# Performance work log

Hardware: AMD Instinct MI355X
Metric: run time of the kernel (lower is better)

## Reference

```python
import jax, jax.numpy as jnp
import numpy as np

KE = 14.3996
R_MAX = 6.0
N_ATOMS = 100000
N_EDGES = 6400000

def _isp(x):
    # inverse softplus on host constants
    return np.log(np.exp(np.asarray(x, np.float64)) - 1.0).astype(np.float32)

def setup_inputs() -> dict:
    key = jax.random.key(0)
    k1, k2, k3 = jax.random.split(key, 3)
    R = jax.random.normal(k1, (N_ATOMS, 3), dtype=jnp.float32) * 10.0
    Z = jax.random.randint(k2, (N_ATOMS,), 1, 50, dtype=jnp.int32)
    idx = jax.random.randint(k3, (2, N_EDGES), 0, N_ATOMS, dtype=jnp.int32)
    return {
        "R": R,
        "Z": Z,
        "idx": idx,
        "a_exp": jnp.full((1,), _isp(0.23)),
        "a_num": jnp.full((1,), _isp(0.4685)),
        "coefficients": jnp.asarray(_isp([0.18175, 0.50986, 0.28022, 0.02817]))[:, None],
        "exponents": jnp.asarray(_isp([3.1998, 0.94229, 0.4029, 0.20162]))[:, None],
        "rep_scale": jnp.full((1,), _isp(1.0 / KE)),
    }

def reference(R, Z, idx, a_exp, a_num, coefficients, exponents, rep_scale):
    idx_i, idx_j = idx[0], idx[1]
    Zf = Z.astype(jnp.float32)
    Z_i = Zf[idx_i]                     # [E]
    Z_j = Zf[idx_j]                     # [E]
    # free-space displacement: Rj - Ri
    dr_vec = R[idx_j] - R[idx_i]        # [E,3]
    dr = jnp.sqrt(jnp.sum(dr_vec * dr_vec, axis=-1))  # [E]
    dr = jnp.clip(dr, 0.02, R_MAX)
    cos_cutoff = 0.5 * (jnp.cos(jnp.pi * dr / R_MAX) + 1.0)
    ae = jax.nn.softplus(a_exp)         # (1,)
    an = jax.nn.softplus(a_num)         # (1,)
    coeffs = jax.nn.softplus(coefficients)  # (4,1)
    exps = jax.nn.softplus(exponents)       # (4,1)
    rs = jax.nn.softplus(rep_scale)     # (1,)
    a_divisor = Z_i ** ae + Z_j ** ae   # [E] (broadcast of (1,))
    dist = dr * a_divisor / an          # [E]
    f = jnp.sum(coeffs * jnp.exp(-exps * dist[None, :]), axis=0)  # [E]
    E_ij = Z_i * Z_j / dr * f * cos_cutoff  # [E]
    mask = (idx_i != idx_j).astype(E_ij.dtype)  # padding mask (self-pairs)
    E_ij = E_ij * mask
    E = 0.5 * rs * KE * jnp.sum(E_ij)
    return jnp.sum(E)
```

## Files before the change

kernel.cpp:

```cpp
#include <hip/hip_runtime.h>
#include <math.h>

#define KE 14.3996f
#define R_MAX 6.0f

#define PSCALE 512.0f
#define INV_PS2 (1.0f / (512.0f * 512.0f))

#define WS_POW_F 16


typedef short s4 __attribute__((ext_vector_type(4)));

__device__ __forceinline__ float softplus_f(float x) { return log1pf(expf(x)); }

__device__ __forceinline__ int bin2(float x) {
    int b = (int)floorf((x + 16.0f) * 0.5f);
    return min(max(b, 0), 15);
}

__global__ __launch_bounds__(256) void atom_prep(
        const float* __restrict__ R, const int* __restrict__ Z,
        const float* __restrict__ a_exp, const float* __restrict__ a_num,
        const float* __restrict__ coef, const float* __restrict__ expo,
        const float* __restrict__ rs,
        unsigned char* __restrict__ XY, unsigned char* __restrict__ Z4,
        unsigned char* __restrict__ X4, s4* __restrict__ P8,
        float* __restrict__ ws, float* __restrict__ out, int nA) {
    const int i = blockIdx.x * 256 + threadIdx.x;
    if (blockIdx.x == 0) {
        const int t = threadIdx.x;
        const float ae = softplus_f(a_exp[0]);
        if (t == 0) {
            ws[0] = ae;
            ws[1] = 1.0f / softplus_f(a_num[0]);
            ws[2] = 0.5f * KE * softplus_f(rs[0]);
            out[0] = 0.0f;
        }
        if (t < 4) { ws[3 + t] = softplus_f(coef[t]); ws[7 + t] = softplus_f(expo[t]); }
        if (t < 64) ws[WS_POW_F + t] = (t > 0) ? expf(ae * logf((float)t)) : 0.0f;
    }
    if (i < nA) {
        const float x = R[3 * i], y = R[3 * i + 1], z = R[3 * i + 2];
        s4 v;
        v.x = (short)lrintf(x * PSCALE);
        v.y = (short)lrintf(y * PSCALE);
        v.z = (short)lrintf(z * PSCALE);
        v.w = (short)Z[i];
        P8[i] = v;
        XY[i] = (unsigned char)(bin2(x) | (bin2(y) << 4));
    }
    if ((i & 1) == 0 && i < nA) {
        unsigned int zb = (unsigned int)bin2(R[3 * i + 2]);
        unsigned int xb = (unsigned int)bin2(R[3 * i]);
        if (i + 1 < nA) {
            zb |= ((unsigned int)bin2(R[3 * (i + 1) + 2])) << 4;
            xb |= ((unsigned int)bin2(R[3 * (i + 1)])) << 4;
        }
        Z4[i >> 1] = (unsigned char)zb;
        X4[i >> 1] = (unsigned char)xb;
    }
}

__device__ __forceinline__ float edge_term(const s4* __restrict__ P8, int i, int j,
                                           const float* __restrict__ R,
                                           const float* __restrict__ spow,
                                           float inv_an,
                                           float c0, float c1, float c2, float c3,
                                           float e0, float e1, float e2, float e3) {
    const s4 pa = P8[i];
    const s4 pb = P8[j];
    const float dx = (float)(pb.x - pa.x);
    const float dy = (float)(pb.y - pa.y);
    const float dz = (float)(pb.z - pa.z);
    const float dr2 = (dx * dx + dy * dy + dz * dz) * INV_PS2;
    if (dr2 >= R_MAX * R_MAX) return 0.0f;
    float dr;
    if (dr2 < 0.1225f) {
        const float ax = R[3 * i], ay = R[3 * i + 1], az = R[3 * i + 2];
        const float bx = R[3 * j], by = R[3 * j + 1], bz = R[3 * j + 2];
        const float fx = bx - ax, fy = by - ay, fz = bz - az;
        dr = fmaxf(__fsqrt_rn(fx * fx + fy * fy + fz * fz), 0.02f);
    } else {
        dr = __fsqrt_rn(dr2);
    }
    const float ppa = spow[(int)pa.w] + spow[(int)pb.w];
    const float dist = dr * ppa * inv_an;
    const float f = c0 * __expf(-e0 * dist) + c1 * __expf(-e1 * dist)
                  + c2 * __expf(-e2 * dist) + c3 * __expf(-e3 * dist);
    const float cut = 0.5f * (__cosf((float)M_PI / R_MAX * dr) + 1.0f);
    return (float)pa.w * (float)pb.w / dr * f * cut;
}

#define QCAP 96

#define PUSH_POP(k_, iv, jv)                                                    \
    {                                                                           \
        const bool _k = (k_);                                                   \
        const unsigned long long _m = __ballot(_k);                             \
        if (_k) {                                                               \
            const int _pos = count + __popcll(_m & ((1ull << lane) - 1));       \
            buf[wv][_pos] = ((unsigned long long)(unsigned int)(iv) << 32)      \
                            | (unsigned int)(jv);                               \
        }                                                                       \
        count += __popcll(_m);                                                  \
        if (count >= 32) {                    \
            const int _kk = (count < 64) ? count : 64;                          \
            count -= _kk;                                                       \
            if (lane < _kk) {                                                   \
                const unsigned long long _p = buf[wv][count + lane];            \
                local += edge_term(P8, (int)(_p >> 32), (int)(_p & 0xffffffffu),\
                                   R, spow, inv_an, c0,c1,c2,c3, e0,e1,e2,e3);  \
            }                                                                   \
        }                                                                       \
    }

#define EDGE_BODY                                                               \
    const float inv_an = ssc[1];                                                \
    const float c0 = ssc[3], c1 = ssc[4], c2 = ssc[5], c3 = ssc[6];             \
    const float e0 = ssc[7], e1 = ssc[8], e2 = ssc[9], e3 = ssc[10];            \
    float local = 0.0f;                                                         \
    int count = 0;                                                              \
    const int wpb = blockDim.x >> 6;                                            \
    const int nW = gridDim.x * wpb;                                             \
    const int nG = (nE + 255) >> 8;                                             \
    for (int g = blockIdx.x * wpb + wv; g < nG; g += nW) {                      \
        const int base = (g << 8) + (lane << 2);                                \
        int4 ii, jj;                                                            \
        bool v0 = false, v1 = false, v2 = false, v3 = false;                    \
        if (base + 3 < nE) {                                                    \
            ii = *(const int4*)(idx_i + base);                                  \
            jj = *(const int4*)(idx_j + base);                                  \
            v0 = v1 = v2 = v3 = true;                                           \
        } else {                                                                \
            ii.x = ii.y = ii.z = ii.w = 0;                                      \
            jj.x = jj.y = jj.z = jj.w = 0;                                      \
            if (base < nE)     { ii.x = idx_i[base];     jj.x = idx_j[base];     v0 = true; } \
            if (base + 1 < nE) { ii.y = idx_i[base + 1]; jj.y = idx_j[base + 1]; v1 = true; } \
            if (base + 2 < nE) { ii.z = idx_i[base + 2]; jj.z = idx_j[base + 2]; v2 = true; } \
        }                                                                       \
        const bool k0 = v0 && keepf(ii.x, jj.x) && (ii.x != jj.x);              \
        const bool k1 = v1 && keepf(ii.y, jj.y) && (ii.y != jj.y);              \
        const bool k2 = v2 && keepf(ii.z, jj.z) && (ii.z != jj.z);              \
        const bool k3 = v3 && keepf(ii.w, jj.w) && (ii.w != jj.w);              \
        PUSH_POP(k0, ii.x, jj.x)                                                \
        PUSH_POP(k1, ii.y, jj.y)                                                \
        PUSH_POP(k2, ii.z, jj.z)                                                \
        PUSH_POP(k3, ii.w, jj.w)                                                \
    }                                                                           \
    while (count > 0) {                                              \
        const int k = (count < 64) ? count : 64;                                \
        count -= k;                                                             \
        if (lane < k) {                                                         \
            const unsigned long long p = buf[wv][count + lane];                 \
            local += edge_term(P8, (int)(p >> 32), (int)(p & 0xffffffffu),      \
                               R, spow, inv_an, c0,c1,c2,c3, e0,e1,e2,e3);      \
        }                                                                       \
    }                                                                           \
    for (int off = 32; off > 0; off >>= 1) local += __shfl_down(local, off);    \
    if (lane == 0) wsum[wv] = local;                                            \
    __syncthreads();                                                            \
    if (threadIdx.x == 0) {                                                     \
        float s = 0.0f;                                                         \
        for (int w = 0; w < (int)(blockDim.x >> 6); ++w) s += wsum[w];          \
        atomicAdd(out, s * ssc[2]);                                             \
    }

__global__ __launch_bounds__(1024) void zbl_big(
        const unsigned char* __restrict__ XY, const unsigned char* __restrict__ Z4,
        const s4* __restrict__ P8, const float* __restrict__ R,
        const int* __restrict__ idx_i, const int* __restrict__ idx_j,
        const float* __restrict__ ws, float* __restrict__ out, int nE, int nA) {
    extern __shared__ unsigned char lds[];
    __shared__ unsigned long long buf[16][QCAP];
    __shared__ float spow[64];
    __shared__ float ssc[11];
    __shared__ float wsum[16];
    const int tid = threadIdx.x, lane = tid & 63, wv = tid >> 6;
    const int xyPad = (nA + 15) & ~15;
    const int z4Pad = (((nA + 1) >> 1) + 15) & ~15;
    for (int off = tid * 16; off < xyPad; off += 1024 * 16)
        *(int4*)(lds + off) = *(const int4*)(XY + off);
    unsigned char* ldsZ = lds + xyPad;
    for (int off = tid * 16; off < z4Pad; off += 1024 * 16)
        *(int4*)(ldsZ + off) = *(const int4*)(Z4 + off);
    if (tid < 64) spow[tid] = ws[WS_POW_F + tid];
    if (tid < 11) ssc[tid] = ws[tid];
    __syncthreads();

    auto keepf = [&](int i, int j) -> bool {
        const unsigned int ci = lds[i], cj = lds[j];
        const unsigned int zi = (ldsZ[i >> 1] >> ((i & 1) * 4)) & 15u;
        const unsigned int zj = (ldsZ[j >> 1] >> ((j & 1) * 4)) & 15u;
        return (abs((int)(ci & 15u) - (int)(cj & 15u)) <= 3)
            && (abs((int)(ci >> 4) - (int)(cj >> 4)) <= 3)
            && (abs((int)zi - (int)zj) <= 3);
    };
    EDGE_BODY
}

__global__ __launch_bounds__(1024) void zbl_safe(
        const unsigned char* __restrict__ X4,
        const s4* __restrict__ P8, const float* __restrict__ R,
        const int* __restrict__ idx_i, const int* __restrict__ idx_j,
        const float* __restrict__ ws, float* __restrict__ out, int nE, int nA) {
    extern __shared__ unsigned char lds[];
    __shared__ unsigned long long buf[16][QCAP];
    __shared__ float spow[64];
    __shared__ float ssc[11];
    __shared__ float wsum[16];
    const int tid = threadIdx.x, lane = tid & 63, wv = tid >> 6;
    const int x4Pad = (((nA + 1) >> 1) + 15) & ~15;
    for (int off = tid * 16; off < x4Pad; off += 1024 * 16)
        *(int4*)(lds + off) = *(const int4*)(X4 + off);
    if (tid < 64) spow[tid] = ws[WS_POW_F + tid];
    if (tid < 11) ssc[tid] = ws[tid];
    __syncthreads();

    auto keepf = [&](int i, int j) -> bool {
        const unsigned int bi = (lds[i >> 1] >> ((i & 1) * 4)) & 15u;
        const unsigned int bj = (lds[j >> 1] >> ((j & 1) * 4)) & 15u;
        return abs((int)bi - (int)bj) <= 3;
    };
    EDGE_BODY
}

extern "C" void kernel_launch(void* const* d_in, const int* in_sizes, int n_in,
                              void* d_out, int out_size, void* d_ws, size_t ws_size,
                              hipStream_t stream) {
    const float* R     = (const float*)d_in[0];
    const int*   Z     = (const int*)d_in[1];
    const int*   idx   = (const int*)d_in[2];
    const float* a_exp = (const float*)d_in[3];
    const float* a_num = (const float*)d_in[4];
    const float* coef  = (const float*)d_in[5];
    const float* expo  = (const float*)d_in[6];
    const float* rs    = (const float*)d_in[7];

    float* out = (float*)d_out;
    float* wsf = (float*)d_ws;
    unsigned char* wsb = (unsigned char*)d_ws;

    const int nA = in_sizes[0] / 3;
    const int nE = in_sizes[2] / 2;
    const int* idx_i = idx;
    const int* idx_j = idx + nE;

    const int xyPad = (nA + 15) & ~15;
    const int nibPad = (((nA + 1) >> 1) + 15) & ~15;
    unsigned char* XY = wsb + 512;
    unsigned char* Z4 = XY + xyPad;
    unsigned char* X4 = Z4 + nibPad;
    s4* P8 = (s4*)(X4 + nibPad);

    atom_prep<<<(nA + 255) / 256, 256, 0, stream>>>(R, Z, a_exp, a_num, coef,
                                                    expo, rs, XY, Z4, X4, P8,
                                                    wsf, out, nA);

    const int dynBig = xyPad + nibPad;
    int dev = 0;
    (void)hipGetDevice(&dev);
    int maxShm = 0;
    (void)hipDeviceGetAttribute(&maxShm, hipDeviceAttributeMaxSharedMemoryPerBlock, dev);
    hipFuncAttributes fa{};
    (void)hipFuncGetAttributes(&fa, (const void*)zbl_big);
    const int staticLds = 16 * QCAP * 8 + 256 + 48 + 64 + 64;
    const bool big = (maxShm >= dynBig + staticLds) ||
                     (fa.maxDynamicSharedSizeBytes >= dynBig);

    if (big) {
        (void)hipFuncSetAttribute((const void*)zbl_big,
                                  hipFuncAttributeMaxDynamicSharedMemorySize, dynBig);
        zbl_big<<<256, 1024, dynBig, stream>>>(XY, Z4, P8, R, idx_i, idx_j,
                                               wsf, out, nE, nA);
    } else {
        zbl_safe<<<512, 1024, nibPad, stream>>>(X4, P8, R, idx_i, idx_j,
                                                wsf, out, nE, nA);
    }
}
```

Baseline: 112.2 us.

## Drop z-bin prefilter, prefetch next edge chunk, flush queue only in full waves

Removes the z-axis coarse-bin test from the LDS prefilter, which cuts the Z4 nibble array, its LDS copy and one pair of LDS lookups per edge. More edges now pass to the exact distance check instead. The edge loop is software-pipelined so the next chunk's index loads are issued before the current chunk is filtered. The compaction queue grows to 128 entries and is drained only when a full wave of 64 pairs is ready, using mbcnt for the lane prefix and branch-free range checks. The risk is more edge_term evaluations from the weaker filter and extra register pressure from the prefetch.

```diff
diff --git a/kernel.cpp b/kernel.cpp
--- a/kernel.cpp
+++ b/kernel.cpp
@@ -24,8 +24,8 @@
         const float* __restrict__ a_exp, const float* __restrict__ a_num,
         const float* __restrict__ coef, const float* __restrict__ expo,
         const float* __restrict__ rs,
-        unsigned char* __restrict__ XY, unsigned char* __restrict__ Z4,
-        unsigned char* __restrict__ X4, s4* __restrict__ P8,
+        unsigned char* __restrict__ XY, unsigned char* __restrict__ X4,
+        s4* __restrict__ P8,
         float* __restrict__ ws, float* __restrict__ out, int nA) {
     const int i = blockIdx.x * 256 + threadIdx.x;
     if (blockIdx.x == 0) {
@@ -51,13 +51,8 @@
         XY[i] = (unsigned char)(bin2(x) | (bin2(y) << 4));
     }
     if ((i & 1) == 0 && i < nA) {
-        unsigned int zb = (unsigned int)bin2(R[3 * i + 2]);
         unsigned int xb = (unsigned int)bin2(R[3 * i]);
-        if (i + 1 < nA) {
-            zb |= ((unsigned int)bin2(R[3 * (i + 1) + 2])) << 4;
-            xb |= ((unsigned int)bin2(R[3 * (i + 1)])) << 4;
-        }
-        Z4[i >> 1] = (unsigned char)zb;
+        if (i + 1 < nA) xb |= ((unsigned int)bin2(R[3 * (i + 1)])) << 4;
         X4[i >> 1] = (unsigned char)xb;
     }
 }
@@ -92,26 +87,40 @@
     return (float)pa.w * (float)pb.w / dr * f * cut;
 }
 
-#define QCAP 96
+#define QCAP 128
 
 #define PUSH_POP(k_, iv, jv)                                                    \
     {                                                                           \
         const bool _k = (k_);                                                   \
         const unsigned long long _m = __ballot(_k);                             \
         if (_k) {                                                               \
-            const int _pos = count + __popcll(_m & ((1ull << lane) - 1));       \
-            buf[wv][_pos] = ((unsigned long long)(unsigned int)(iv) << 32)      \
+            const int _pfx = (int)__builtin_amdgcn_mbcnt_hi(                    \
+                (unsigned int)(_m >> 32),                                       \
+                __builtin_amdgcn_mbcnt_lo((unsigned int)_m, 0u));               \
+            buf[wv][count + _pfx] = ((unsigned long long)(unsigned int)(iv) << 32) \
                             | (unsigned int)(jv);                               \
         }                                                                       \
         count += __popcll(_m);                                                  \
-        if (count >= 32) {                    \
-            const int _kk = (count < 64) ? count : 64;                          \
-            count -= _kk;                                                       \
-            if (lane < _kk) {                                                   \
-                const unsigned long long _p = buf[wv][count + lane];            \
-                local += edge_term(P8, (int)(_p >> 32), (int)(_p & 0xffffffffu),\
-                                   R, spow, inv_an, c0,c1,c2,c3, e0,e1,e2,e3);  \
-            }                                                                   \
+        if (count >= 64) {            \
+            count -= 64;                                                        \
+            const unsigned long long _p = buf[wv][count + lane];                \
+            local += edge_term(P8, (int)(_p >> 32), (int)(_p & 0xffffffffu),    \
+                               R, spow, inv_an, c0,c1,c2,c3, e0,e1,e2,e3);      \
+        }                                                                       \
+    }
+
+#define LOADQ(g_, ii_, jj_)                                                     \
+    {                                                                           \
+        const int _b = ((g_) << 8) + (lane << 2);                               \
+        if (_b + 3 < nE) {                                                      \
+            ii_ = *(const int4*)(idx_i + _b);                                   \
+            jj_ = *(const int4*)(idx_j + _b);                                   \
+        } else {                                                                \
+            ii_.x = ii_.y = ii_.z = ii_.w = 0;                                  \
+            jj_.x = jj_.y = jj_.z = jj_.w = 0;                                  \
+            if (_b < nE)     { ii_.x = idx_i[_b];     jj_.x = idx_j[_b]; }      \
+            if (_b + 1 < nE) { ii_.y = idx_i[_b + 1]; jj_.y = idx_j[_b + 1]; }  \
+            if (_b + 2 < nE) { ii_.z = idx_i[_b + 2]; jj_.z = idx_j[_b + 2]; }  \
         }                                                                       \
     }
 
@@ -124,29 +133,25 @@
     const int wpb = blockDim.x >> 6;                                            \
     const int nW = gridDim.x * wpb;                                             \
     const int nG = (nE + 255) >> 8;                                             \
-    for (int g = blockIdx.x * wpb + wv; g < nG; g += nW) {                      \
-        const int base = (g << 8) + (lane << 2);                                \
+    int g = blockIdx.x * wpb + wv;                                              \
+    if (g < nG) {                                                               \
         int4 ii, jj;                                                            \
-        bool v0 = false, v1 = false, v2 = false, v3 = false;                    \
-        if (base + 3 < nE) {                                                    \
-            ii = *(const int4*)(idx_i + base);                                  \
-            jj = *(const int4*)(idx_j + base);                                  \
-            v0 = v1 = v2 = v3 = true;                                           \
-        } else {                                                                \
-            ii.x = ii.y = ii.z = ii.w = 0;                                      \
-            jj.x = jj.y = jj.z = jj.w = 0;                                      \
-            if (base < nE)     { ii.x = idx_i[base];     jj.x = idx_j[base];     v0 = true; } \
-            if (base + 1 < nE) { ii.y = idx_i[base + 1]; jj.y = idx_j[base + 1]; v1 = true; } \
-            if (base + 2 < nE) { ii.z = idx_i[base + 2]; jj.z = idx_j[base + 2]; v2 = true; } \
-        }                                                                       \
-        const bool k0 = v0 && keepf(ii.x, jj.x) && (ii.x != jj.x);              \
-        const bool k1 = v1 && keepf(ii.y, jj.y) && (ii.y != jj.y);              \
-        const bool k2 = v2 && keepf(ii.z, jj.z) && (ii.z != jj.z);              \
-        const bool k3 = v3 && keepf(ii.w, jj.w) && (ii.w != jj.w);              \
-        PUSH_POP(k0, ii.x, jj.x)                                                \
-        PUSH_POP(k1, ii.y, jj.y)                                                \
-        PUSH_POP(k2, ii.z, jj.z)                                                \
-        PUSH_POP(k3, ii.w, jj.w)                                                \
+        LOADQ(g, ii, jj)                                                        \
+        while (true) {                                                          \
+            const int gn = g + nW;                                              \
+            int4 iin, jjn;                                                      \
+            if (gn < nG) LOADQ(gn, iin, jjn)                                    \
+            const bool k0 = (ii.x != jj.x) && keepf(ii.x, jj.x);                \
+            const bool k1 = (ii.y != jj.y) && keepf(ii.y, jj.y);                \
+            const bool k2 = (ii.z != jj.z) && keepf(ii.z, jj.z);                \
+            const bool k3 = (ii.w != jj.w) && keepf(ii.w, jj.w);                \
+            PUSH_POP(k0, ii.x, jj.x)                                            \
+            PUSH_POP(k1, ii.y, jj.y)                                            \
+            PUSH_POP(k2, ii.z, jj.z)                                            \
+            PUSH_POP(k3, ii.w, jj.w)                                            \
+            if (gn >= nG) break;                                                \
+            g = gn; ii = iin; jj = jjn;                                         \
+        }                                                                       \
     }                                                                           \
     while (count > 0) {                                              \
         const int k = (count < 64) ? count : 64;                                \
@@ -167,7 +172,7 @@
     }
 
 __global__ __launch_bounds__(1024) void zbl_big(
-        const unsigned char* __restrict__ XY, const unsigned char* __restrict__ Z4,
+        const unsigned char* __restrict__ XY,
         const s4* __restrict__ P8, const float* __restrict__ R,
         const int* __restrict__ idx_i, const int* __restrict__ idx_j,
         const float* __restrict__ ws, float* __restrict__ out, int nE, int nA) {
@@ -178,23 +183,16 @@
     __shared__ float wsum[16];
     const int tid = threadIdx.x, lane = tid & 63, wv = tid >> 6;
     const int xyPad = (nA + 15) & ~15;
-    const int z4Pad = (((nA + 1) >> 1) + 15) & ~15;
     for (int off = tid * 16; off < xyPad; off += 1024 * 16)
         *(int4*)(lds + off) = *(const int4*)(XY + off);
-    unsigned char* ldsZ = lds + xyPad;
-    for (int off = tid * 16; off < z4Pad; off += 1024 * 16)
-        *(int4*)(ldsZ + off) = *(const int4*)(Z4 + off);
     if (tid < 64) spow[tid] = ws[WS_POW_F + tid];
     if (tid < 11) ssc[tid] = ws[tid];
     __syncthreads();
 
     auto keepf = [&](int i, int j) -> bool {
-        const unsigned int ci = lds[i], cj = lds[j];
-        const unsigned int zi = (ldsZ[i >> 1] >> ((i & 1) * 4)) & 15u;
-        const unsigned int zj = (ldsZ[j >> 1] >> ((j & 1) * 4)) & 15u;
-        return (abs((int)(ci & 15u) - (int)(cj & 15u)) <= 3)
-            && (abs((int)(ci >> 4) - (int)(cj >> 4)) <= 3)
-            && (abs((int)zi - (int)zj) <= 3);
+        const int ci = lds[i], cj = lds[j];
+        return ((unsigned)((ci & 15) - (cj & 15) + 3) <= 6u)
+             & ((unsigned)((ci >> 4) - (cj >> 4) + 3) <= 6u);
     };
     EDGE_BODY
 }
@@ -218,9 +216,9 @@
     __syncthreads();
 
     auto keepf = [&](int i, int j) -> bool {
-        const unsigned int bi = (lds[i >> 1] >> ((i & 1) * 4)) & 15u;
-        const unsigned int bj = (lds[j >> 1] >> ((j & 1) * 4)) & 15u;
-        return abs((int)bi - (int)bj) <= 3;
+        const int bi = (lds[i >> 1] >> ((i & 1) * 4)) & 15;
+        const int bj = (lds[j >> 1] >> ((j & 1) * 4)) & 15;
+        return (unsigned)(bi - bj + 3) <= 6u;
     };
     EDGE_BODY
 }
@@ -249,15 +247,14 @@
     const int xyPad = (nA + 15) & ~15;
     const int nibPad = (((nA + 1) >> 1) + 15) & ~15;
     unsigned char* XY = wsb + 512;
-    unsigned char* Z4 = XY + xyPad;
-    unsigned char* X4 = Z4 + nibPad;
+    unsigned char* X4 = XY + xyPad;
     s4* P8 = (s4*)(X4 + nibPad);
 
     atom_prep<<<(nA + 255) / 256, 256, 0, stream>>>(R, Z, a_exp, a_num, coef,
-                                                    expo, rs, XY, Z4, X4, P8,
+                                                    expo, rs, XY, X4, P8,
                                                     wsf, out, nA);
 
-    const int dynBig = xyPad + nibPad;
+    const int dynBig = xyPad;
     int dev = 0;
     (void)hipGetDevice(&dev);
     int maxShm = 0;
@@ -271,7 +268,7 @@
     if (big) {
         (void)hipFuncSetAttribute((const void*)zbl_big,
                                   hipFuncAttributeMaxDynamicSharedMemorySize, dynBig);
-        zbl_big<<<256, 1024, dynBig, stream>>>(XY, Z4, P8, R, idx_i, idx_j,
+        zbl_big<<<256, 1024, dynBig, stream>>>(XY, P8, R, idx_i, idx_j,
                                                wsf, out, nE, nA);
     } else {
         zbl_safe<<<512, 1024, nibPad, stream>>>(X4, P8, R, idx_i, idx_j,
```

New measurement: 112.5 us. No clear change (+0.4%).
